# Kernel optimization log

Measured on AMD Instinct MI355X. Metric: run time of the kernel, lower is better.

Reference implementation:

```python
import jax, jax.numpy as jnp
import numpy as np

B, NP, C_IN, H = 8, 6250, 512, 256   # graphs, nodes/graph, in-feat, hidden
EPG = 100000                          # edges per graph
K = 5000                              # ceil(0.8 * NP) kept by TopKPooling
H3 = 3 * H


def setup_inputs() -> dict:
    key = jax.random.key(0)
    ks = jax.random.split(key, 16)
    N, E = B * NP, B * EPG
    x = jax.random.normal(ks[0], (N, C_IN), jnp.float32)
    offs = (jnp.arange(E) // EPG) * NP  # keep edges inside their graph
    src = jax.random.randint(ks[1], (E,), 0, NP) + offs
    dst = jax.random.randint(ks[2], (E,), 0, NP) + offs
    edge_index = jnp.stack([src, dst]).astype(jnp.int64)
    edge_attr = jax.random.uniform(ks[3], (E,), jnp.float32)
    batch = jnp.repeat(jnp.arange(B), NP).astype(jnp.int64)
    s = 0.05
    W1 = jax.random.normal(ks[4], (C_IN, H), jnp.float32) * s
    b1 = jnp.zeros((H,), jnp.float32)
    W2 = jax.random.normal(ks[5], (H, H), jnp.float32) * s
    b2 = jnp.zeros((H,), jnp.float32)
    pw = jax.random.normal(ks[6], (H3,), jnp.float32) * s   # TopKPooling attn vector
    lw1 = jax.random.normal(ks[7], (H3 * 2, H), jnp.float32) * s
    lb1 = jnp.zeros((H,), jnp.float32)
    lw2 = jax.random.normal(ks[8], (H, H // 2), jnp.float32) * s
    lb2 = jnp.zeros((H // 2,), jnp.float32)
    lw3 = jax.random.normal(ks[9], (H // 2, 3), jnp.float32) * s
    lb3 = jnp.zeros((3,), jnp.float32)
    return {"x": x, "edge_index": edge_index, "edge_attr": edge_attr, "batch": batch,
            "W1": W1, "b1": b1, "W2": W2, "b2": b2, "pw": pw,
            "lw1": lw1, "lb1": lb1, "lw2": lw2, "lb2": lb2, "lw3": lw3, "lb3": lb3}


def _gcn(x, W, b, src, dst, ew, n):
    xw = x @ W
    deg = jnp.zeros((n,), xw.dtype).at[dst].add(ew) + 1.0
    dinv = jax.lax.rsqrt(deg)
    norm = dinv[src] * ew * dinv[dst]
    out = jnp.zeros_like(xw).at[dst].add(norm[:, None] * xw[src])
    return out + (dinv * dinv)[:, None] * xw + b


def reference(x, edge_index, edge_attr, batch, W1, b1, W2, b2, pw,
              lw1, lb1, lw2, lb2, lw3, lb3):
    N = x.shape[0]
    src, dst = edge_index[0], edge_index[1]
    x1 = jax.nn.relu(_gcn(x, W1, b1, src, dst, edge_attr, N))
    x2 = jax.nn.relu(_gcn(x1, W2, b2, src, dst, edge_attr, N))
    x3 = jax.nn.relu(_gcn(x2, W2, b2, src, dst, edge_attr, N))  # conv2 reused (as in source)
    cat_x = jnp.concatenate([x1, x2, x3], axis=1)               # [N, 3H]
    # TopKPooling: score = sigmoid((x . w) / ||w||), keep top-K per graph, scale by score
    score = jax.nn.sigmoid((cat_x @ pw) / jnp.linalg.norm(pw))   # [N]
    sc = score.reshape(B, NP)
    topv, topi = jax.lax.top_k(sc, K)                            # [B, K]
    xg = cat_x.reshape(B, NP, H3)
    sel = jnp.take_along_axis(xg, topi[:, :, None], axis=1) * topv[:, :, None]  # [B, K, 3H]
    readout = jnp.concatenate([sel.mean(axis=1), sel.max(axis=1)], axis=1)      # [B, 6H]
    h = jax.nn.relu(readout @ lw1 + lb1)
    h = jax.nn.relu(h @ lw2 + lb2)       # dropout p=0 is a no-op
    return h @ lw3 + lb3                 # [B, 3]
```

## Files before the change

### kernel.cpp

```cpp
#include <hip/hip_runtime.h>
#include <stdint.h>

#define NODES  50000
#define MPAD   50048
#define NGRAPH 8
#define NP_G   6250
#define EPG    100000
#define EDGES  800000
#define KKEEP  5000
#define HID    256
#define CIN    512
#define H3     768
#define SCANB  196
#define RCHUNK 200
#define MLPCH  24
#define MLPCK  64
#define ESL    3125

#define K1_HIST  512
#define K1_W1    512
#define K1_W2    256
#define K1_TOTAL (K1_HIST + K1_W1 + K1_W2 + 1)
#define GEMM_GRID 784
#define FILL_GRID 256

using f32x4  = __attribute__((ext_vector_type(4))) float;
using bf16x8 = __attribute__((ext_vector_type(8))) short;
using u16x8  = __attribute__((ext_vector_type(8))) unsigned short;
typedef unsigned short u16;
typedef unsigned int   u32;
typedef unsigned long long u64;

__device__ __forceinline__ float bf2f(u16 u) {
    return __uint_as_float(((uint32_t)u) << 16);
}
__device__ __forceinline__ u16 f2bf(float f) {
    uint32_t u = __float_as_uint(f);
    u += 0x7fffu + ((u >> 16) & 1u);
    return (u16)(u >> 16);
}
__device__ __forceinline__ int4 f32x8_to_bf16x8(float4 a, float4 b) {
    int4 r;
    asm("v_cvt_pk_bf16_f32 %0, %1, %2" : "=v"(r.x) : "v"(a.x), "v"(a.y));
    asm("v_cvt_pk_bf16_f32 %0, %1, %2" : "=v"(r.y) : "v"(a.z), "v"(a.w));
    asm("v_cvt_pk_bf16_f32 %0, %1, %2" : "=v"(r.z) : "v"(b.x), "v"(b.y));
    asm("v_cvt_pk_bf16_f32 %0, %1, %2" : "=v"(r.w) : "v"(b.z), "v"(b.w));
    return r;
}

__global__ __launch_bounds__(256) void k1_kernel(
        const int* __restrict__ ei, const float* __restrict__ ew,
        u64* __restrict__ partial,
        const float* __restrict__ W1, const float* __restrict__ W2,
        const float* __restrict__ pw,
        u16* __restrict__ Wt1, u16* __restrict__ Wt2, float* __restrict__ invn) {
    __shared__ __align__(16) char smem[ESL * 8];
    int b = blockIdx.x, t = threadIdx.x;
    if (b < K1_HIST) {
        u64* hl = (u64*)smem;
        int g  = b >> 6;
        int r  = b & 63;
        int bb = r >> 1;
        int h  = r & 1;
        for (int k = t; k < ESL; k += 256) hl[k] = 0ull;
        __syncthreads();
        int ebase = g * EPG + bb * ESL;
        int lo = h * ESL;
        for (int k = t; k < ESL; k += 256) {
            int e = ebase + k;
            int d = ei[EDGES + e];
            int il = d - g * NP_G - lo;
            if ((unsigned)il < (unsigned)ESL) {
                u64 enc = (1ull << 48) | (u64)(ew[e] * 4294967296.0f);
                atomicAdd(&hl[il], enc);
            }
        }
        __syncthreads();
        u64* prow = partial + (size_t)(g * 32 + bb) * NP_G + lo;
        for (int k = t; k < ESL; k += 256) prow[k] = hl[k];
    } else if (b < K1_HIST + K1_W1) {
        int id = (b - K1_HIST) * 256 + t;
        int n = id >> 9, k = id & 511;
        Wt1[id] = f2bf(W1[(size_t)k * HID + n]);
    } else if (b < K1_TOTAL - 1) {
        int id = (b - K1_HIST - K1_W1) * 256 + t;
        int n = id >> 8, k = id & 255;
        Wt2[id] = f2bf(W2[(size_t)k * HID + n]);
    } else {
        float* sh = (float*)smem;
        float s = 0.f;
        for (int i = t; i < H3; i += 256) { float v = pw[i]; s += v * v; }
        sh[t] = s; __syncthreads();
        for (int off = 128; off; off >>= 1) {
            if (t < off) sh[t] += sh[t + off];
            __syncthreads();
        }
        if (t == 0) invn[0] = rsqrtf(sh[0]);
    }
}

__global__ void scan1_kernel(const u64* __restrict__ partial,
                             u32* __restrict__ blockbase,
                             int* __restrict__ iscan, int* __restrict__ bsum,
                             float* __restrict__ dinv) {
    int b = blockIdx.x, t = threadIdx.x;
    int i = b * 256 + t;
    int c = 0;
    if (i < NODES) {
        int g = i / NP_G, il = i - g * NP_G;
        size_t base = (size_t)(g * 32) * NP_G + il;
        u64 fix = 0ull; u32 cnt = 0;
#pragma unroll 4
        for (int j = 0; j < 32; ++j) {
            size_t idx = base + (size_t)j * NP_G;
            u64 pv = partial[idx];
            blockbase[idx] = cnt;
            cnt += (u32)(pv >> 48);
            fix += pv & 0xFFFFFFFFFFFFull;
        }
        c = (int)cnt;
        float deg = (float)fix * (1.0f / 4294967296.0f);
        dinv[i] = rsqrtf(deg + 1.0f);
    }
    int lane = t & 63, wv = t >> 6;
    int v = c;
    for (int off = 1; off < 64; off <<= 1) {
        int u = __shfl_up(v, off);
        if (lane >= off) v += u;
    }
    __shared__ int ws[4];
    if (lane == 63) ws[wv] = v;
    __syncthreads();
    if (t == 0) { int s = 0; for (int k = 0; k < 4; k++) { int tmp = ws[k]; ws[k] = s; s += tmp; } }
    __syncthreads();
    v += ws[wv];
    if (i < NODES) iscan[i] = v - c;
    if (t == 255) bsum[b] = v;
}

__global__ void scan3_kernel(const int* __restrict__ iscan, const int* __restrict__ bsum,
                             int* __restrict__ rowptr) {
    int b = blockIdx.x, t = threadIdx.x;
    int v = (t < b) ? bsum[t] : 0;
    for (int off = 1; off < 64; off <<= 1) v += __shfl_xor(v, off, 64);
    __shared__ int ws[4];
    if ((t & 63) == 0) ws[t >> 6] = v;
    __syncthreads();
    int boffb = ws[0] + ws[1] + ws[2] + ws[3];
    int i = b * 256 + t;
    if (i > NODES) return;
    if (i == NODES) { rowptr[NODES] = EDGES; return; }
    rowptr[i] = boffb + iscan[i];
}

__device__ __forceinline__ bool gemm_map(int i, int& bm, int& bn) {
    int g = i & 7, s = i >> 3;
    int cnt = (g == 5) ? 48 : 49;
    if ((s >> 1) >= cnt) return false;
    bm = 49 * g - (g > 5 ? 1 : 0) + (s >> 1);
    bn = s & 1;
    return true;
}

__device__ __forceinline__ void gemm_body(const u16* __restrict__ A,
                                          const u16* __restrict__ Bt,
                                          u16* __restrict__ C,
                                          int K, int bm, int bn,
                                          u16* As, u16* Bs) {
    const int tid  = threadIdx.x;
    const int wave = tid >> 6, lane = tid & 63;
    const int wm = wave >> 1, wn = wave & 1;
    const int quad = lane >> 4, l16 = lane & 15;
    const int sr = tid >> 2;
    const int sc = tid & 3;
    const int swz = (sc ^ ((sr >> 1) & 3)) * 8;
    const int rphys = (quad ^ ((l16 >> 1) & 3)) * 8;

    const u16* Ag = A + (size_t)(bm * 128 + sr) * K + sc * 8;
    const u16* Bg = Bt + (size_t)(bn * 128 + sr) * K + sc * 8;

    f32x4 acc[4][4];
#pragma unroll
    for (int i = 0; i < 4; i++)
#pragma unroll
        for (int j = 0; j < 4; j++) { f32x4 z = {0.f, 0.f, 0.f, 0.f}; acc[i][j] = z; }

    for (int k0 = 0; k0 < K; k0 += 32) {
        int4 av0 = *(const int4*)(Ag + k0);
        int4 av1 = *(const int4*)(Ag + (size_t)64 * K + k0);
        int4 bv0 = *(const int4*)(Bg + k0);
        int4 bv1 = *(const int4*)(Bg + (size_t)64 * K + k0);
        __syncthreads();
        *(int4*)(As + sr * 32 + swz)        = av0;
        *(int4*)(As + (sr + 64) * 32 + swz) = av1;
        *(int4*)(Bs + sr * 32 + swz)        = bv0;
        *(int4*)(Bs + (sr + 64) * 32 + swz) = bv1;
        __syncthreads();
        bf16x8 af[4], bfr[4];
#pragma unroll
        for (int i = 0; i < 4; i++)
            af[i] = *(const bf16x8*)(As + (wm * 64 + i * 16 + l16) * 32 + rphys);
#pragma unroll
        for (int j = 0; j < 4; j++)
            bfr[j] = *(const bf16x8*)(Bs + (wn * 64 + j * 16 + l16) * 32 + rphys);
#pragma unroll
        for (int i = 0; i < 4; i++)
#pragma unroll
            for (int j = 0; j < 4; j++)
                acc[i][j] = __builtin_amdgcn_mfma_f32_16x16x32_bf16(af[i], bfr[j], acc[i][j], 0, 0, 0);
    }

    const int crow0 = bm * 128 + wm * 64 + quad * 4;
    const int ccol0 = bn * 128 + wn * 64 + l16;
#pragma unroll
    for (int i = 0; i < 4; i++)
#pragma unroll
        for (int j = 0; j < 4; j++)
#pragma unroll
            for (int r = 0; r < 4; r++)
                C[(size_t)(crow0 + i * 16 + r) * HID + ccol0 + j * 16] = f2bf(acc[i][j][r]);
}

__global__ __launch_bounds__(256) void k2_kernel(
        const float* __restrict__ X, const u16* __restrict__ Wt1,
        u16* __restrict__ C) {
    __shared__ u16 As[128 * 32];
    __shared__ u16 Bs[128 * 32];
    int bm, bn;
    if (!gemm_map(blockIdx.x, bm, bn)) return;

    const int tid  = threadIdx.x;
    const int wave = tid >> 6, lane = tid & 63;
    const int wm = wave >> 1, wn = wave & 1;
    const int quad = lane >> 4, l16 = lane & 15;
    const int sr = tid >> 2;
    const int sc = tid & 3;
    const int swz = (sc ^ ((sr >> 1) & 3)) * 8;
    const int rphys = (quad ^ ((l16 >> 1) & 3)) * 8;

    int r0 = bm * 128 + sr;      if (r0 > NODES - 1) r0 = NODES - 1;
    int r1 = bm * 128 + sr + 64; if (r1 > NODES - 1) r1 = NODES - 1;
    const float* Ag0 = X + (size_t)r0 * CIN + sc * 8;
    const float* Ag1 = X + (size_t)r1 * CIN + sc * 8;
    const u16*   Bg  = Wt1 + (size_t)(bn * 128 + sr) * CIN + sc * 8;

    f32x4 acc[4][4];
#pragma unroll
    for (int i = 0; i < 4; i++)
#pragma unroll
        for (int j = 0; j < 4; j++) { f32x4 z = {0.f, 0.f, 0.f, 0.f}; acc[i][j] = z; }

    for (int k0 = 0; k0 < CIN; k0 += 32) {
        float4 a00 = *(const float4*)(Ag0 + k0);
        float4 a01 = *(const float4*)(Ag0 + k0 + 4);
        float4 a10 = *(const float4*)(Ag1 + k0);
        float4 a11 = *(const float4*)(Ag1 + k0 + 4);
        int4 bv0 = *(const int4*)(Bg + k0);
        int4 bv1 = *(const int4*)(Bg + (size_t)64 * CIN + k0);
        int4 av0 = f32x8_to_bf16x8(a00, a01);
        int4 av1 = f32x8_to_bf16x8(a10, a11);
        __syncthreads();
        *(int4*)(As + sr * 32 + swz)        = av0;
        *(int4*)(As + (sr + 64) * 32 + swz) = av1;
        *(int4*)(Bs + sr * 32 + swz)        = bv0;
        *(int4*)(Bs + (sr + 64) * 32 + swz) = bv1;
        __syncthreads();
        bf16x8 af[4], bfr[4];
#pragma unroll
        for (int i = 0; i < 4; i++)
            af[i] = *(const bf16x8*)(As + (wm * 64 + i * 16 + l16) * 32 + rphys);
#pragma unroll
        for (int j = 0; j < 4; j++)
            bfr[j] = *(const bf16x8*)(Bs + (wn * 64 + j * 16 + l16) * 32 + rphys);
#pragma unroll
        for (int i = 0; i < 4; i++)
#pragma unroll
            for (int j = 0; j < 4; j++)
                acc[i][j] = __builtin_amdgcn_mfma_f32_16x16x32_bf16(af[i], bfr[j], acc[i][j], 0, 0, 0);
    }

    const int crow0 = bm * 128 + wm * 64 + quad * 4;
    const int ccol0 = bn * 128 + wn * 64 + l16;
#pragma unroll
    for (int i = 0; i < 4; i++)
#pragma unroll
        for (int j = 0; j < 4; j++)
#pragma unroll
            for (int r = 0; r < 4; r++)
                C[(size_t)(crow0 + i * 16 + r) * HID + ccol0 + j * 16] = f2bf(acc[i][j][r]);
}

__global__ __launch_bounds__(256) void fill_kernel(
        const int* __restrict__ ei, const float* __restrict__ ew,
        const float* __restrict__ dinv, const int* __restrict__ rowptr,
        const u32* __restrict__ blockbase, int2* __restrict__ csr) {
    __shared__ u32 cursor[ESL];
    int g  = blockIdx.x & 7;
    int bb = blockIdx.x >> 3;
    const u32* bbase = blockbase + (size_t)(g * 32 + bb) * NP_G;
    const int* rp = rowptr + g * NP_G;
    int ebase = g * EPG + bb * ESL;
    for (int h = 0; h < 2; ++h) {
        int lo = h * ESL;
        for (int k = threadIdx.x; k < ESL; k += 256)
            cursor[k] = (u32)rp[lo + k] + bbase[lo + k];
        __syncthreads();
#pragma unroll 4
        for (int k = threadIdx.x; k < ESL; k += 256) {
            int e = ebase + k;
            int d = ei[EDGES + e];
            int il = d - g * NP_G - lo;
            if ((unsigned)il < (unsigned)ESL) {
                int s = ei[e];
                u32 pos = atomicAdd(&cursor[il], 1u);
                csr[pos] = make_int2(s, __float_as_int(dinv[s] * ew[e] * dinv[d]));
            }
        }
        __syncthreads();
    }
}

__global__ __launch_bounds__(256) void gemm_bt(const u16* __restrict__ A,
                                               const u16* __restrict__ Bt,
                                               u16* __restrict__ C, int K) {
    __shared__ u16 As[128 * 32];
    __shared__ u16 Bs[128 * 32];
    int bm, bn;
    if (!gemm_map(blockIdx.x, bm, bn)) return;
    gemm_body(A, Bt, C, K, bm, bn, As, Bs);
}

template<bool SCORE>
__global__ void agg_kernel(const u16* __restrict__ xw, u16* __restrict__ xo,
                           const int* __restrict__ rowptr, const int2* __restrict__ csr,
                           const float* __restrict__ dinv, const float* __restrict__ bias,
                           const u16* __restrict__ xs1, const u16* __restrict__ xs2,
                           const float* __restrict__ pw, const float* __restrict__ invn,
                           float* __restrict__ score, u64* __restrict__ keys) {
    int wave = threadIdx.x >> 6;
    int lane = threadIdx.x & 63;
    int g  = blockIdx.x & 7;
    int nl = (blockIdx.x >> 3) * 4 + wave;
    if (nl >= NP_G) return;
    int w = g * NP_G + nl;
    int half = lane >> 5;
    int f8 = (lane & 31) * 8;
    size_t ro = (size_t)w * HID + f8;

    float acc0[8], acc1[8];
#pragma unroll
    for (int j = 0; j < 8; ++j) { acc0[j] = 0.f; acc1[j] = 0.f; }

    int p = rowptr[w], p1 = rowptr[w + 1];
    for (int q = p; q < p1; q += 64) {
        int m = min(64, p1 - q);
        int2 e = make_int2(0, 0);
        if (lane < m) e = csr[q + lane];
        int j = 0;
        for (; j + 8 <= m; j += 8) {
            int i0 = j + half,     i1 = j + 2 + half;
            int i2 = j + 4 + half, i3 = j + 6 + half;
            int   s0 = __shfl(e.x, i0, 64); float w0 = __int_as_float(__shfl(e.y, i0, 64));
            int   s1 = __shfl(e.x, i1, 64); float w1 = __int_as_float(__shfl(e.y, i1, 64));
            int   s2 = __shfl(e.x, i2, 64); float w2 = __int_as_float(__shfl(e.y, i2, 64));
            int   s3 = __shfl(e.x, i3, 64); float w3 = __int_as_float(__shfl(e.y, i3, 64));
            u16x8 v0 = *(const u16x8*)(xw + (size_t)s0 * HID + f8);
            u16x8 v1 = *(const u16x8*)(xw + (size_t)s1 * HID + f8);
            u16x8 v2 = *(const u16x8*)(xw + (size_t)s2 * HID + f8);
            u16x8 v3 = *(const u16x8*)(xw + (size_t)s3 * HID + f8);
#pragma unroll
            for (int t = 0; t < 8; ++t) {
                acc0[t] += w0 * bf2f(v0[t]);
                acc1[t] += w1 * bf2f(v1[t]);
                acc0[t] += w2 * bf2f(v2[t]);
                acc1[t] += w3 * bf2f(v3[t]);
            }
        }
        for (; j + 2 <= m; j += 2) {
            int i0 = j + half;
            int s0 = __shfl(e.x, i0, 64); float w0 = __int_as_float(__shfl(e.y, i0, 64));
            u16x8 v0 = *(const u16x8*)(xw + (size_t)s0 * HID + f8);
#pragma unroll
            for (int t = 0; t < 8; ++t) acc0[t] += w0 * bf2f(v0[t]);
        }
        if (j < m) {
            int s0 = __shfl(e.x, j, 64); float w0 = __int_as_float(__shfl(e.y, j, 64));
            w0 = half ? 0.f : w0;
            u16x8 v0 = *(const u16x8*)(xw + (size_t)s0 * HID + f8);
#pragma unroll
            for (int t = 0; t < 8; ++t) acc0[t] += w0 * bf2f(v0[t]);
        }
    }

#pragma unroll
    for (int j = 0; j < 8; ++j) {
        acc0[j] += acc1[j];
        acc0[j] += __shfl(acc0[j], lane ^ 32, 64);
    }

    float di = dinv[w], sw = di * di;
    u16x8 sv = *(const u16x8*)(xw + ro);
    float bb[8];
    {
        float4 t0 = *(const float4*)(bias + f8);
        float4 t1 = *(const float4*)(bias + f8 + 4);
        bb[0] = t0.x; bb[1] = t0.y; bb[2] = t0.z; bb[3] = t0.w;
        bb[4] = t1.x; bb[5] = t1.y; bb[6] = t1.z; bb[7] = t1.w;
    }
    u16x8 o;
    float ov[8];
#pragma unroll
    for (int j = 0; j < 8; ++j) {
        float v = fmaxf(acc0[j] + sw * bf2f(sv[j]) + bb[j], 0.f);
        o[j] = f2bf(v);
        ov[j] = bf2f(o[j]);
    }
    if (half == 0) *(u16x8*)(xo + ro) = o;

    if (SCORE) {
        u16x8 v1 = *(const u16x8*)(xs1 + ro);
        u16x8 v2 = *(const u16x8*)(xs2 + ro);
        float acc = 0.f;
#pragma unroll
        for (int j = 0; j < 8; ++j) {
            acc += bf2f(v1[j]) * pw[f8 + j];
            acc += bf2f(v2[j]) * pw[256 + f8 + j];
            acc += ov[j]       * pw[512 + f8 + j];
        }
#pragma unroll
        for (int off = 1; off < 32; off <<= 1) acc += __shfl_xor(acc, off, 64);
        if (lane == 0) {
            float s = acc * invn[0];
            float sc = 1.f / (1.f + __expf(-s));
            score[w] = sc;
            keys[w] = ((u64)__float_as_uint(sc) << 13) | (unsigned int)(NP_G - 1 - nl);
        }
    }
}

__global__ __launch_bounds__(1024) void selcomp_kernel(
        const u64* __restrict__ keys, const float* __restrict__ score,
        int* __restrict__ selidx, float* __restrict__ selscr) {
    __shared__ u64 kk[NP_G];
    __shared__ unsigned int hist[4][256];
    __shared__ unsigned int sfx[257];
    __shared__ u64 spref;
    __shared__ unsigned int swant;
    int g = blockIdx.x, t = threadIdx.x;
    const u64* kg = keys + (size_t)g * NP_G;
    for (int i = t; i < NP_G; i += 1024) kk[i] = kg[i];
    if (t == 0) { spref = 0ull; swant = KKEEP; }
    const int wgrp = (t >> 8) & 3;
    u64 mask = 0ull;
    __syncthreads();
    for (int shift = 40; shift >= 0; shift -= 8) {
        if (t < 256) { hist[0][t] = 0; hist[1][t] = 0; hist[2][t] = 0; hist[3][t] = 0; }
        __syncthreads();
        u64 pref = spref;
        for (int i = t; i < NP_G; i += 1024) {
            u64 key = kk[i];
            if ((key & mask) == pref)
                atomicAdd(&hist[wgrp][(unsigned int)(key >> shift) & 255u], 1u);
        }
        __syncthreads();
        if (t < 256) sfx[t] = hist[0][t] + hist[1][t] + hist[2][t] + hist[3][t];
        if (t == 0) sfx[256] = 0;
        __syncthreads();
        for (int off = 1; off < 256; off <<= 1) {
            unsigned int v = 0;
            if (t < 256 && t + off < 256) v = sfx[t + off];
            __syncthreads();
            if (t < 256 && t + off < 256) sfx[t] += v;
            __syncthreads();
        }
        unsigned int want = swant;
        __syncthreads();
        if (t < 256) {
            unsigned int s0 = sfx[t], s1 = sfx[t + 1];
            if (s0 >= want && s1 < want) {
                spref = pref | ((u64)t << shift);
                swant = want - s1;
            }
        }
        __syncthreads();
        mask |= (255ull << shift);
    }
    u64 kth = spref;
    int lane = t & 63, wv = t >> 6;
    __shared__ int wsum[16];
    __shared__ int cbase;
    if (t == 0) cbase = 0;
    __syncthreads();
    for (int k = 0; k < (NP_G + 1023) / 1024; ++k) {
        int i = k * 1024 + t;
        bool sel = (i < NP_G) && (kk[i] >= kth);
        int n = g * NP_G + i;
        u64 bal = __ballot(sel);
        int prefix = __popcll(bal & ((1ull << lane) - 1ull));
        if (lane == 0) wsum[wv] = __popcll(bal);
        __syncthreads();
        if (t == 0) {
            int s = cbase;
            for (int j = 0; j < 16; ++j) { int tmp = wsum[j]; wsum[j] = s; s += tmp; }
            cbase = s;
        }
        __syncthreads();
        if (sel) {
            int pos = wsum[wv] + prefix;
            selidx[g * KKEEP + pos] = n;
            selscr[g * KKEEP + pos] = score[n];
        }
        __syncthreads();
    }
}

__global__ __launch_bounds__(256) void readout_kernel(
        const u16* __restrict__ x1, const u16* __restrict__ x2,
        const u16* __restrict__ x3,
        const int* __restrict__ selidx, const float* __restrict__ selscr,
        float* __restrict__ sumbuf, int* __restrict__ maxbuf) {
    int g = blockIdx.x, tpart = blockIdx.y, c = blockIdx.z;
    int fcol = threadIdx.x;
    const u16* xt = (tpart == 0) ? x1 : ((tpart == 1) ? x2 : x3);
    __shared__ int   sidx[RCHUNK];
    __shared__ float sscr[RCHUNK];
    int base = g * KKEEP + c * RCHUNK;
    if (fcol < RCHUNK) { sidx[fcol] = selidx[base + fcol]; sscr[fcol] = selscr[base + fcol]; }
    __syncthreads();
    float sum = 0.f, mx = 0.f;
#pragma unroll 1
    for (int j = 0; j < RCHUNK; j += 4) {
        int n0 = sidx[j], n1 = sidx[j + 1], n2 = sidx[j + 2], n3 = sidx[j + 3];
        float s0 = sscr[j], s1 = sscr[j + 1], s2 = sscr[j + 2], s3 = sscr[j + 3];
        float v0 = bf2f(xt[(size_t)n0 * HID + fcol]) * s0;
        float v1 = bf2f(xt[(size_t)n1 * HID + fcol]) * s1;
        float v2 = bf2f(xt[(size_t)n2 * HID + fcol]) * s2;
        float v3 = bf2f(xt[(size_t)n3 * HID + fcol]) * s3;
        sum += v0 + v1 + v2 + v3;
        mx = fmaxf(mx, fmaxf(fmaxf(v0, v1), fmaxf(v2, v3)));
    }
    int o = (g * 3 + tpart) * HID + fcol;
    atomicAdd(&sumbuf[o], sum);
    atomicMax(&maxbuf[o], __float_as_int(mx));
}

__global__ __launch_bounds__(256) void mlp1_kernel(const float* __restrict__ sumbuf,
                                                   const int* __restrict__ maxbuf,
                                                   const float* __restrict__ lw1,
                                                   float* __restrict__ h1acc) {
    int g = blockIdx.x, ch = blockIdx.y, t = threadIdx.x;
    __shared__ float r[MLPCK];
    int k0 = ch * MLPCK;
    if (t < MLPCK) {
        int i = k0 + t;
        r[t] = (i < 768) ? sumbuf[g * 768 + i] * (1.f / 5000.f)
                         : __int_as_float(maxbuf[g * 768 + (i - 768)]);
    }
    __syncthreads();
    float a0 = 0.f, a1 = 0.f, a2 = 0.f, a3 = 0.f;
#pragma unroll
    for (int i = 0; i < MLPCK; i += 4) {
        a0 += r[i]     * lw1[(size_t)(k0 + i)     * 256 + t];
        a1 += r[i + 1] * lw1[(size_t)(k0 + i + 1) * 256 + t];
        a2 += r[i + 2] * lw1[(size_t)(k0 + i + 2) * 256 + t];
        a3 += r[i + 3] * lw1[(size_t)(k0 + i + 3) * 256 + t];
    }
    atomicAdd(&h1acc[g * 256 + t], (a0 + a1) + (a2 + a3));
}

__global__ __launch_bounds__(256) void mlp2_kernel(const float* __restrict__ h1acc,
                                                   const float* __restrict__ lb1,
                                                   const float* __restrict__ lw2,
                                                   const float* __restrict__ lb2,
                                                   const float* __restrict__ lw3,
                                                   const float* __restrict__ lb3,
                                                   float* __restrict__ out) {
    __shared__ float h1[256];
    __shared__ float part[256];
    __shared__ float h2[128];
    int g = blockIdx.x, t = threadIdx.x;
    h1[t] = fmaxf(h1acc[g * 256 + t] + lb1[t], 0.f);
    __syncthreads();
    int col = t & 127, half = t >> 7;
    float a = 0.f;
#pragma unroll
    for (int i = 0; i < 128; i += 4) {
        int k = half * 128 + i;
        a += h1[k]     * lw2[k * 128 + col]
           + h1[k + 1] * lw2[(k + 1) * 128 + col]
           + h1[k + 2] * lw2[(k + 2) * 128 + col]
           + h1[k + 3] * lw2[(k + 3) * 128 + col];
    }
    part[t] = a;
    __syncthreads();
    if (t < 128) h2[t] = fmaxf(part[t] + part[t + 128] + lb2[t], 0.f);
    __syncthreads();
    if (t < 3) {
        float a3 = lb3[t];
        for (int i = 0; i < 128; ++i) a3 += h2[i] * lw3[i * 3 + t];
        out[g * 3 + t] = a3;
    }
}

extern "C" void kernel_launch(void* const* d_in, const int* in_sizes, int n_in,
                              void* d_out, int out_size, void* d_ws, size_t ws_size,
                              hipStream_t stream) {
    const float* x   = (const float*)d_in[0];
    const int*   ei  = (const int*)d_in[1];
    const float* ew  = (const float*)d_in[2];
    const float* W1  = (const float*)d_in[4];
    const float* b1  = (const float*)d_in[5];
    const float* W2  = (const float*)d_in[6];
    const float* b2  = (const float*)d_in[7];
    const float* pw  = (const float*)d_in[8];
    const float* lw1 = (const float*)d_in[9];
    const float* lb1 = (const float*)d_in[10];
    const float* lw2 = (const float*)d_in[11];
    const float* lb2 = (const float*)d_in[12];
    const float* lw3 = (const float*)d_in[13];
    const float* lb3 = (const float*)d_in[14];
    float* out = (float*)d_out;

    char* p = (char*)d_ws;
    auto alloc = [&](size_t bytes) -> char* {
        char* r = p;
        p += (bytes + 255) & ~(size_t)255;
        return r;
    };
    u16* A0  = (u16*)alloc((size_t)MPAD * CIN * 2);
    u16* x3  = (u16*)alloc((size_t)MPAD * HID * 2);
    u16* xw  = (u16*)alloc((size_t)MPAD * HID * 2);
    u16* Wt1 = (u16*)alloc((size_t)HID * CIN * 2);
    u16* Wt2 = (u16*)alloc((size_t)HID * HID * 2);
    int2*  csr    = (int2*)alloc((size_t)EDGES * 8);
    u64*   partial   = (u64*)alloc((size_t)256 * NP_G * 8);
    u32*   blockbase = (u32*)alloc((size_t)256 * NP_G * 4);
    int*   rowptr = (int*)alloc((size_t)(NODES + 1) * 4);
    int*   iscan  = (int*)alloc((size_t)NODES * 4);
    int*   bsum   = (int*)alloc((size_t)SCANB * 4);
    u64*   keys   = (u64*)alloc((size_t)NODES * 8);
    float* score  = (float*)alloc((size_t)NODES * 4);
    float* dinv   = (float*)alloc((size_t)NODES * 4);
    int*   selidx = (int*)alloc((size_t)NGRAPH * KKEEP * 4);
    float* selscr = (float*)alloc((size_t)NGRAPH * KKEEP * 4);
    float* invn   = (float*)alloc(256);
    char* zbase = p;
    float* sumbuf = (float*)alloc(6144 * 4);
    int*   maxbuf = (int*)alloc(6144 * 4);
    float* h1acc  = (float*)alloc((size_t)NGRAPH * 256 * 4);
    size_t zbytes = (size_t)(p - zbase);

    u16* x1 = A0;
    u16* x2 = A0 + (size_t)MPAD * HID;

    hipMemsetAsync(zbase, 0, zbytes, stream);

    k1_kernel<<<K1_TOTAL, 256, 0, stream>>>(ei, ew, partial,
                                            W1, W2, pw, Wt1, Wt2, invn);
    scan1_kernel<<<SCANB, 256, 0, stream>>>(partial, blockbase, iscan, bsum, dinv);
    scan3_kernel<<<SCANB + 1, 256, 0, stream>>>(iscan, bsum, rowptr);
    k2_kernel<<<GEMM_GRID, 256, 0, stream>>>(x, Wt1, xw);
    fill_kernel<<<FILL_GRID, 256, 0, stream>>>(ei, ew, dinv, rowptr, blockbase, csr);

    int aggBlocks = 8 * ((NP_G + 3) / 4);

    agg_kernel<false><<<aggBlocks, 256, 0, stream>>>(xw, x1, rowptr, csr, dinv, b1,
                                                     nullptr, nullptr, nullptr, nullptr,
                                                     nullptr, nullptr);
    gemm_bt<<<GEMM_GRID, 256, 0, stream>>>(x1, Wt2, xw, HID);
    agg_kernel<false><<<aggBlocks, 256, 0, stream>>>(xw, x2, rowptr, csr, dinv, b2,
                                                     nullptr, nullptr, nullptr, nullptr,
                                                     nullptr, nullptr);
    gemm_bt<<<GEMM_GRID, 256, 0, stream>>>(x2, Wt2, xw, HID);
    agg_kernel<true><<<aggBlocks, 256, 0, stream>>>(xw, x3, rowptr, csr, dinv, b2,
                                                    x1, x2, pw, invn, score, keys);

    selcomp_kernel<<<NGRAPH, 1024, 0, stream>>>(keys, score, selidx, selscr);
    readout_kernel<<<dim3(NGRAPH, 3, KKEEP / RCHUNK), 256, 0, stream>>>(
        x1, x2, x3, selidx, selscr, sumbuf, maxbuf);
    mlp1_kernel<<<dim3(NGRAPH, MLPCH), 256, 0, stream>>>(sumbuf, maxbuf, lw1, h1acc);
    mlp2_kernel<<<NGRAPH, 256, 0, stream>>>(h1acc, lb1, lw2, lb2, lw3, lb3, out);
}
```

Baseline: 475.7 us.

## Load GEMM MFMA operands directly from global memory, dropping LDS staging

Both the fp32-input first-layer GEMM and the bf16 GEMM now use one templated body in which each wave loads its MFMA fragments straight from global memory into registers. The shared-memory tiles and both __syncthreads per k-step are gone, and the k loop is unrolled 4x. This removes LDS traffic and barrier stalls. In exchange, each wave re-reads A and B rows that other waves share, which relies on L2/L1 hits, and the per-lane 16-byte strided row loads are less coalesced.

```diff
diff --git a/kernel.cpp b/kernel.cpp
--- a/kernel.cpp
+++ b/kernel.cpp
@@ -39,13 +39,13 @@
     u += 0x7fffu + ((u >> 16) & 1u);
     return (u16)(u >> 16);
 }
-__device__ __forceinline__ int4 f32x8_to_bf16x8(float4 a, float4 b) {
+__device__ __forceinline__ bf16x8 f32x8_to_bf16x8(float4 a, float4 b) {
     int4 r;
     asm("v_cvt_pk_bf16_f32 %0, %1, %2" : "=v"(r.x) : "v"(a.x), "v"(a.y));
     asm("v_cvt_pk_bf16_f32 %0, %1, %2" : "=v"(r.y) : "v"(a.z), "v"(a.w));
     asm("v_cvt_pk_bf16_f32 %0, %1, %2" : "=v"(r.z) : "v"(b.x), "v"(b.y));
     asm("v_cvt_pk_bf16_f32 %0, %1, %2" : "=v"(r.w) : "v"(b.z), "v"(b.w));
-    return r;
+    return __builtin_bit_cast(bf16x8, r);
 }
 
 __global__ __launch_bounds__(256) void k1_kernel(
@@ -162,22 +162,30 @@
     return true;
 }
 
-__device__ __forceinline__ void gemm_body(const u16* __restrict__ A,
-                                          const u16* __restrict__ Bt,
-                                          u16* __restrict__ C,
-                                          int K, int bm, int bn,
-                                          u16* As, u16* Bs) {
+template<bool F32A>
+__device__ __forceinline__ void gemm_stream(const void* __restrict__ Aptr,
+                                            const u16* __restrict__ Bt,
+                                            u16* __restrict__ C,
+                                            int K, int bm, int bn) {
     const int tid  = threadIdx.x;
     const int wave = tid >> 6, lane = tid & 63;
     const int wm = wave >> 1, wn = wave & 1;
     const int quad = lane >> 4, l16 = lane & 15;
-    const int sr = tid >> 2;
-    const int sc = tid & 3;
-    const int swz = (sc ^ ((sr >> 1) & 3)) * 8;
-    const int rphys = (quad ^ ((l16 >> 1) & 3)) * 8;
-
-    const u16* Ag = A + (size_t)(bm * 128 + sr) * K + sc * 8;
-    const u16* Bg = Bt + (size_t)(bn * 128 + sr) * K + sc * 8;
+
+    const float* Af = (const float*)Aptr;
+    const u16*   Ah = (const u16*)Aptr;
+
+    const float* Afp[4];
+    const u16*   Ahp[4];
+    const u16*   Bp[4];
+#pragma unroll
+    for (int i = 0; i < 4; i++) {
+        int r = bm * 128 + wm * 64 + i * 16 + l16;
+        if (F32A && r > NODES - 1) r = NODES - 1;
+        if (F32A) Afp[i] = Af + (size_t)r * K + quad * 8;
+        else      Ahp[i] = Ah + (size_t)r * K + quad * 8;
+        Bp[i] = Bt + (size_t)(bn * 128 + wn * 64 + i * 16 + l16) * K + quad * 8;
+    }
 
     f32x4 acc[4][4];
 #pragma unroll
@@ -185,29 +193,27 @@
 #pragma unroll
         for (int j = 0; j < 4; j++) { f32x4 z = {0.f, 0.f, 0.f, 0.f}; acc[i][j] = z; }
 
+#pragma unroll 4
     for (int k0 = 0; k0 < K; k0 += 32) {
-        int4 av0 = *(const int4*)(Ag + k0);
-        int4 av1 = *(const int4*)(Ag + (size_t)64 * K + k0);
-        int4 bv0 = *(const int4*)(Bg + k0);
-        int4 bv1 = *(const int4*)(Bg + (size_t)64 * K + k0);
-        __syncthreads();
-        *(int4*)(As + sr * 32 + swz)        = av0;
-        *(int4*)(As + (sr + 64) * 32 + swz) = av1;
-        *(int4*)(Bs + sr * 32 + swz)        = bv0;
-        *(int4*)(Bs + (sr + 64) * 32 + swz) = bv1;
-        __syncthreads();
-        bf16x8 af[4], bfr[4];
+        bf16x8 av[4], bv[4];
+#pragma unroll
+        for (int i = 0; i < 4; i++) {
+            if (F32A) {
+                float4 p = *(const float4*)(Afp[i] + k0);
+                float4 q = *(const float4*)(Afp[i] + k0 + 4);
+                av[i] = f32x8_to_bf16x8(p, q);
+            } else {
+                av[i] = *(const bf16x8*)(Ahp[i] + k0);
+            }
+        }
+#pragma unroll
+        for (int j = 0; j < 4; j++)
+            bv[j] = *(const bf16x8*)(Bp[j] + k0);
 #pragma unroll
         for (int i = 0; i < 4; i++)
-            af[i] = *(const bf16x8*)(As + (wm * 64 + i * 16 + l16) * 32 + rphys);
-#pragma unroll
-        for (int j = 0; j < 4; j++)
-            bfr[j] = *(const bf16x8*)(Bs + (wn * 64 + j * 16 + l16) * 32 + rphys);
-#pragma unroll
-        for (int i = 0; i < 4; i++)
 #pragma unroll
             for (int j = 0; j < 4; j++)
-                acc[i][j] = __builtin_amdgcn_mfma_f32_16x16x32_bf16(af[i], bfr[j], acc[i][j], 0, 0, 0);
+                acc[i][j] = __builtin_amdgcn_mfma_f32_16x16x32_bf16(av[i], bv[j], acc[i][j], 0, 0, 0);
     }
 
     const int crow0 = bm * 128 + wm * 64 + quad * 4;
@@ -224,70 +230,17 @@
 __global__ __launch_bounds__(256) void k2_kernel(
         const float* __restrict__ X, const u16* __restrict__ Wt1,
         u16* __restrict__ C) {
-    __shared__ u16 As[128 * 32];
-    __shared__ u16 Bs[128 * 32];
     int bm, bn;
     if (!gemm_map(blockIdx.x, bm, bn)) return;
-
-    const int tid  = threadIdx.x;
-    const int wave = tid >> 6, lane = tid & 63;
-    const int wm = wave >> 1, wn = wave & 1;
-    const int quad = lane >> 4, l16 = lane & 15;
-    const int sr = tid >> 2;
-    const int sc = tid & 3;
-    const int swz = (sc ^ ((sr >> 1) & 3)) * 8;
-    const int rphys = (quad ^ ((l16 >> 1) & 3)) * 8;
-
-    int r0 = bm * 128 + sr;      if (r0 > NODES - 1) r0 = NODES - 1;
-    int r1 = bm * 128 + sr + 64; if (r1 > NODES - 1) r1 = NODES - 1;
-    const float* Ag0 = X + (size_t)r0 * CIN + sc * 8;
-    const float* Ag1 = X + (size_t)r1 * CIN + sc * 8;
-    const u16*   Bg  = Wt1 + (size_t)(bn * 128 + sr) * CIN + sc * 8;
-
-    f32x4 acc[4][4];
-#pragma unroll
-    for (int i = 0; i < 4; i++)
-#pragma unroll
-        for (int j = 0; j < 4; j++) { f32x4 z = {0.f, 0.f, 0.f, 0.f}; acc[i][j] = z; }
-
-    for (int k0 = 0; k0 < CIN; k0 += 32) {
-        float4 a00 = *(const float4*)(Ag0 + k0);
-        float4 a01 = *(const float4*)(Ag0 + k0 + 4);
-        float4 a10 = *(const float4*)(Ag1 + k0);
-        float4 a11 = *(const float4*)(Ag1 + k0 + 4);
-        int4 bv0 = *(const int4*)(Bg + k0);
-        int4 bv1 = *(const int4*)(Bg + (size_t)64 * CIN + k0);
-        int4 av0 = f32x8_to_bf16x8(a00, a01);
-        int4 av1 = f32x8_to_bf16x8(a10, a11);
-        __syncthreads();
-        *(int4*)(As + sr * 32 + swz)        = av0;
-        *(int4*)(As + (sr + 64) * 32 + swz) = av1;
-        *(int4*)(Bs + sr * 32 + swz)        = bv0;
-        *(int4*)(Bs + (sr + 64) * 32 + swz) = bv1;
-        __syncthreads();
-        bf16x8 af[4], bfr[4];
-#pragma unroll
-        for (int i = 0; i < 4; i++)
-            af[i] = *(const bf16x8*)(As + (wm * 64 + i * 16 + l16) * 32 + rphys);
-#pragma unroll
-        for (int j = 0; j < 4; j++)
-            bfr[j] = *(const bf16x8*)(Bs + (wn * 64 + j * 16 + l16) * 32 + rphys);
-#pragma unroll
-        for (int i = 0; i < 4; i++)
-#pragma unroll
-            for (int j = 0; j < 4; j++)
-                acc[i][j] = __builtin_amdgcn_mfma_f32_16x16x32_bf16(af[i], bfr[j], acc[i][j], 0, 0, 0);
-    }
-
-    const int crow0 = bm * 128 + wm * 64 + quad * 4;
-    const int ccol0 = bn * 128 + wn * 64 + l16;
-#pragma unroll
-    for (int i = 0; i < 4; i++)
-#pragma unroll
-        for (int j = 0; j < 4; j++)
-#pragma unroll
-            for (int r = 0; r < 4; r++)
-                C[(size_t)(crow0 + i * 16 + r) * HID + ccol0 + j * 16] = f2bf(acc[i][j][r]);
+    gemm_stream<true>(X, Wt1, C, CIN, bm, bn);
+}
+
+__global__ __launch_bounds__(256) void gemm_bt(const u16* __restrict__ A,
+                                               const u16* __restrict__ Bt,
+                                               u16* __restrict__ C, int K) {
+    int bm, bn;
+    if (!gemm_map(blockIdx.x, bm, bn)) return;
+    gemm_stream<false>(A, Bt, C, K, bm, bn);
 }
 
 __global__ __launch_bounds__(256) void fill_kernel(
@@ -318,16 +271,6 @@
         }
         __syncthreads();
     }
-}
-
-__global__ __launch_bounds__(256) void gemm_bt(const u16* __restrict__ A,
-                                               const u16* __restrict__ Bt,
-                                               u16* __restrict__ C, int K) {
-    __shared__ u16 As[128 * 32];
-    __shared__ u16 Bs[128 * 32];
-    int bm, bn;
-    if (!gemm_map(blockIdx.x, bm, bn)) return;
-    gemm_body(A, Bt, C, K, bm, bn, As, Bs);
 }
 
 template<bool SCORE>
```

After: 558.5 us. 17.4% more time.
